# Kernel optimization log

Hardware: AMD Instinct MI355X
Metric: run time of the kernel (lower is better)

Reference implementation:

```python
import jax, jax.numpy as jnp
import numpy as np

N, E = 20000, 320000
IN_F, EF, H, C = 2, 1, 128, 2
BN_S = 1.0 / float(np.sqrt(1.0 + 1e-5))  # eval-mode BatchNorm1d with running mean 0, var 1


def _gated_gcn_conv(h, e, src, dst, p, act, residual):
    # DGL GatedGCNConv: e' = C e + D h_src + E h_dst;
    # h' = A h + sum_{in-edges} sigmoid(e') * B h_src / (sum sigmoid(e') + 1e-6)
    Aw, Ab, Bw, Bb, Cw, Cb, Dw, Db, Ew, Eb, bhg, bhb, beg, beb = p
    h_in, e_in = h, e
    Ah = h @ Aw + Ab
    Bh = h @ Bw + Bb
    Dh = h @ Dw + Db
    Eh = h @ Ew + Eb
    e2 = e @ Cw + Cb + Dh[src] + Eh[dst]          # [E, H]
    sig = jax.nn.sigmoid(e2)
    num = jax.ops.segment_sum(sig * Bh[src], dst, num_segments=N)  # [N, H]
    den = jax.ops.segment_sum(sig, dst, num_segments=N)            # [N, H]
    h2 = Ah + num / (den + 1e-6)
    # BatchNorm (eval): (x - 0)/sqrt(1 + eps) * gamma + beta
    h2 = bhg * (h2 * BN_S) + bhb
    e2 = beg * (e2 * BN_S) + beb
    h2, e2 = act(h2), act(e2)
    if residual:
        h2 = h2 + h_in
        e2 = e2 + e_in
    return h2, e2


def _forward(node_feats, edge_feats, src, dst, P):
    (a0_w, a0_b, b0_w, b0_b, c0_w, c0_b, d0_w, d0_b, e0_w, e0_b,
     bnh0_g, bnh0_b, bne0_g, bne0_b,
     aL_w, aL_b, bL_w, bL_b, cL_w, cL_b, dL_w, dL_b, eL_w, eL_b,
     bnhL_g, bnhL_b, bneL_g, bneL_b,
     mlp_w1, mlp_b1, mlp_w2, mlp_b2) = P
    h, e = node_feats, edge_feats
    # layer 0: elu inside conv, residual off (2->128, 1->128)
    p0 = (a0_w, a0_b, b0_w, b0_b, c0_w, c0_b, d0_w, d0_b, e0_w, e0_b,
          bnh0_g, bnh0_b, bne0_g, bne0_b)
    h, e = _gated_gcn_conv(h, e, src, dst, p0, jax.nn.elu, residual=False)
    h = jax.nn.leaky_relu(h)
    e = jax.nn.leaky_relu(e)
    # layers 1..2: leaky_relu inside conv, residual on (128->128)
    for l in range(2):
        pl = (aL_w[l], aL_b[l], bL_w[l], bL_b[l], cL_w[l], cL_b[l],
              dL_w[l], dL_b[l], eL_w[l], eL_b[l],
              bnhL_g[l], bnhL_b[l], bneL_g[l], bneL_b[l])
        h, e = _gated_gcn_conv(h, e, src, dst, pl, jax.nn.leaky_relu, residual=True)
        h = jax.nn.leaky_relu(h)
        e = jax.nn.leaky_relu(e)
    # edge classifier: gather endpoints, concat with edge feats, MLP
    edge_repr = jnp.concatenate([h[src], h[dst], e], axis=1)  # [E, 3H]
    hid = jax.nn.relu(edge_repr @ mlp_w1 + mlp_b1)
    return hid @ mlp_w2 + mlp_b2                               # [E, C]


PARAM_NAMES = ["a0_w", "a0_b", "b0_w", "b0_b", "c0_w", "c0_b", "d0_w", "d0_b",
               "e0_w", "e0_b", "bnh0_g", "bnh0_b", "bne0_g", "bne0_b",
               "aL_w", "aL_b", "bL_w", "bL_b", "cL_w", "cL_b", "dL_w", "dL_b",
               "eL_w", "eL_b", "bnhL_g", "bnhL_b", "bneL_g", "bneL_b",
               "mlp_w1", "mlp_b1", "mlp_w2", "mlp_b2"]


def setup_inputs() -> dict:
    key = jax.random.key(0)
    ks = iter(jax.random.split(key, 64))
    nrm = lambda shp: jax.random.normal(next(ks), shp, dtype=jnp.float32) * 0.05
    inp = {}
    inp["node_feats"] = jax.random.normal(next(ks), (N, IN_F), dtype=jnp.float32)
    inp["edge_feats"] = jax.random.normal(next(ks), (E, EF), dtype=jnp.float32)
    inp["src"] = jax.random.randint(next(ks), (E,), 0, N, dtype=jnp.int32)
    inp["dst"] = jax.random.randint(next(ks), (E,), 0, N, dtype=jnp.int32)
    # layer 0 linears (A,B,D,E: in->H; C: edge->H), biases zero-init like common practice
    for nm, din in [("a0", IN_F), ("b0", IN_F), ("c0", EF), ("d0", IN_F), ("e0", IN_F)]:
        inp[nm + "_w"] = nrm((din, H))
        inp[nm + "_b"] = nrm((H,))
    inp["bnh0_g"] = jnp.ones((H,), jnp.float32)
    inp["bnh0_b"] = jnp.zeros((H,), jnp.float32)
    inp["bne0_g"] = jnp.ones((H,), jnp.float32)
    inp["bne0_b"] = jnp.zeros((H,), jnp.float32)
    # layers 1..2 stacked
    for nm in ["aL", "bL", "cL", "dL", "eL"]:
        inp[nm + "_w"] = nrm((2, H, H))
        inp[nm + "_b"] = nrm((2, H))
    inp["bnhL_g"] = jnp.ones((2, H), jnp.float32)
    inp["bnhL_b"] = jnp.zeros((2, H), jnp.float32)
    inp["bneL_g"] = jnp.ones((2, H), jnp.float32)
    inp["bneL_b"] = jnp.zeros((2, H), jnp.float32)
    # edge MLP
    inp["mlp_w1"] = nrm((3 * H, H))
    inp["mlp_b1"] = nrm((H,))
    inp["mlp_w2"] = nrm((H, C))
    inp["mlp_b2"] = nrm((C,))
    return inp


def reference(node_feats, edge_feats, src, dst,
              a0_w, a0_b, b0_w, b0_b, c0_w, c0_b, d0_w, d0_b, e0_w, e0_b,
              bnh0_g, bnh0_b, bne0_g, bne0_b,
              aL_w, aL_b, bL_w, bL_b, cL_w, cL_b, dL_w, dL_b, eL_w, eL_b,
              bnhL_g, bnhL_b, bneL_g, bneL_b,
              mlp_w1, mlp_b1, mlp_w2, mlp_b2):
    P = (a0_w, a0_b, b0_w, b0_b, c0_w, c0_b, d0_w, d0_b, e0_w, e0_b,
         bnh0_g, bnh0_b, bne0_g, bne0_b,
         aL_w, aL_b, bL_w, bL_b, cL_w, cL_b, dL_w, dL_b, eL_w, eL_b,
         bnhL_g, bnhL_b, bneL_g, bneL_b,
         mlp_w1, mlp_b1, mlp_w2, mlp_b2)
    return _forward(node_feats, edge_feats, src, dst, P)
```

## Files before the change

kernel.cpp:

```cpp
#include <hip/hip_runtime.h>
#include <hip/hip_bf16.h>
#include <math.h>

#define NN 20000
#define NE 320000
#define H 128
#define NH (NN * H)

typedef short bf16x8 __attribute__((ext_vector_type(8)));
typedef float f32x4 __attribute__((ext_vector_type(4)));
typedef unsigned short u16x8 __attribute__((ext_vector_type(8)));

__device__ __forceinline__ float lrelu(float x) { return x > 0.f ? x : 0.01f * x; }
__device__ __forceinline__ float eluf(float x)  { return x > 0.f ? x : expm1f(x); }
__device__ __forceinline__ float sigf(float x)  { return 1.f / (1.f + __expf(-x)); }
__device__ __forceinline__ unsigned short f2b(float x) {
    __hip_bfloat16 h = __float2bfloat16(x);
    return *reinterpret_cast<unsigned short*>(&h);
}
__device__ __forceinline__ float b2f(unsigned short u) {
    __hip_bfloat16 h = *reinterpret_cast<__hip_bfloat16*>(&u);
    return __bfloat162float(h);
}
#define BN_S 0.99999500003749973f

struct PackPtrs { const float* w[13]; };
__global__ __launch_bounds__(256) void k_pack(PackPtrs p, unsigned short* __restrict__ dst) {
    int gid = blockIdx.x * 256 + threadIdx.x;
    int m = gid >> 11;
    int r = gid & 2047;
    int t = r >> 8, kk = (r >> 6) & 3, lane = r & 63;
    const float* W = p.w[m];
    int col = t * 16 + (lane & 15);
    int krow = kk * 32 + (lane >> 4) * 8;
    unsigned short* o = dst + (size_t)m * 16384 + (size_t)r * 8;
#pragma unroll
    for (int j = 0; j < 8; ++j) o[j] = f2b(W[(krow + j) * H + col]);
}

__global__ __launch_bounds__(256) void k_deg(const int* __restrict__ dst, int* __restrict__ deg) {
    int e = blockIdx.x * 256 + threadIdx.x;
    if (e < NE) atomicAdd(&deg[dst[e]], 1);
}

__global__ __launch_bounds__(256) void k_scan(const int* __restrict__ deg,
                                              int* __restrict__ off, int* __restrict__ cursor) {
    __shared__ int sums[256];
    const int t = threadIdx.x;
    const int per = (NN + 255) / 256;
    const int base = t * per;
    int s = 0;
    for (int i = 0; i < per; ++i) { int idx = base + i; if (idx < NN) s += deg[idx]; }
    sums[t] = s;
    __syncthreads();
    for (int d = 1; d < 256; d <<= 1) {
        int v = (t >= d) ? sums[t - d] : 0;
        __syncthreads();
        sums[t] += v;
        __syncthreads();
    }
    int run = (t == 0) ? 0 : sums[t - 1];
    for (int i = 0; i < per; ++i) {
        int idx = base + i;
        if (idx < NN) { off[idx] = run; cursor[idx] = run; run += deg[idx]; }
    }
}

__global__ __launch_bounds__(256) void k_fill(const int* __restrict__ dst,
                                              int* __restrict__ cursor, int* __restrict__ csr) {
    int e = blockIdx.x * 256 + threadIdx.x;
    if (e < NE) {
        int pos = atomicAdd(&cursor[dst[e]], 1);
        csr[pos] = e;
    }
}

__global__ __launch_bounds__(256) void k_seqs(const int* __restrict__ csr,
                                              const int* __restrict__ src,
                                              const int* __restrict__ dst,
                                              int* __restrict__ srcseq,
                                              int* __restrict__ dstseq) {
    int pos = blockIdx.x * 256 + threadIdx.x;
    if (pos < NE) {
        int eid = csr[pos];
        srcseq[pos] = src[eid];
        dstseq[pos] = dst[eid];
    }
}

__global__ __launch_bounds__(256) void k_nodelin0(
        const float* __restrict__ nf,
        const float* __restrict__ wa, const float* __restrict__ ba,
        const float* __restrict__ wb, const float* __restrict__ bb,
        const float* __restrict__ wd, const float* __restrict__ bd,
        const float* __restrict__ we, const float* __restrict__ be,
        float* __restrict__ lin) {
    int idx = blockIdx.x * 256 + threadIdx.x;
    int n = idx >> 7, c = idx & 127;
    float x0 = nf[n * 2], x1 = nf[n * 2 + 1];
    lin[0 * NH + idx] = fmaf(x0, wa[c], fmaf(x1, wa[128 + c], ba[c]));
    lin[1 * NH + idx] = fmaf(x0, wb[c], fmaf(x1, wb[128 + c], bb[c]));
    lin[2 * NH + idx] = fmaf(x0, wd[c], fmaf(x1, wd[128 + c], bd[c]));
    lin[3 * NH + idx] = fmaf(x0, we[c], fmaf(x1, we[128 + c], be[c]));
}

__global__ __launch_bounds__(256) void k_edge0(
        const float* __restrict__ ef,
        const float* __restrict__ cw, const float* __restrict__ cb,
        const int* __restrict__ src, const int* __restrict__ dst,
        const float* __restrict__ lin,
        const float* __restrict__ g, const float* __restrict__ bt,
        unsigned short* __restrict__ ebuf) {
    const int tid = threadIdx.x;
    const int e  = blockIdx.x * 8 + (tid >> 5);
    const int c0 = (tid & 31) * 4;
    const int s = src[e], d = dst[e];
    const float ev = ef[e];
    const float4 cw4 = *(const float4*)(cw + c0);
    const float4 cb4 = *(const float4*)(cb + c0);
    const float4 Dh  = *(const float4*)(lin + 2 * NH + (size_t)s * H + c0);
    const float4 Eh  = *(const float4*)(lin + 3 * NH + (size_t)d * H + c0);
    const float4 g4  = *(const float4*)(g + c0);
    const float4 bt4 = *(const float4*)(bt + c0);
    float e2[4] = { fmaf(ev, cw4.x, cb4.x) + Dh.x + Eh.x,
                    fmaf(ev, cw4.y, cb4.y) + Dh.y + Eh.y,
                    fmaf(ev, cw4.z, cb4.z) + Dh.z + Eh.z,
                    fmaf(ev, cw4.w, cb4.w) + Dh.w + Eh.w };
    const float gg[4] = { g4.x, g4.y, g4.z, g4.w };
    const float bb[4] = { bt4.x, bt4.y, bt4.z, bt4.w };
    ushort4 u;
    u.x = f2b(lrelu(eluf(fmaf(gg[0], e2[0] * BN_S, bb[0]))));
    u.y = f2b(lrelu(eluf(fmaf(gg[1], e2[1] * BN_S, bb[1]))));
    u.z = f2b(lrelu(eluf(fmaf(gg[2], e2[2] * BN_S, bb[2]))));
    u.w = f2b(lrelu(eluf(fmaf(gg[3], e2[3] * BN_S, bb[3]))));
    *(ushort4*)(ebuf + (size_t)e * H + c0) = u;
}

__global__ __launch_bounds__(256) void k_agg0(
        const int* __restrict__ off, const int* __restrict__ deg,
        const int* __restrict__ csr, const int* __restrict__ srcseq,
        const float* __restrict__ ef, const float* __restrict__ cw, const float* __restrict__ cb,
        const float* __restrict__ lin,
        const float* __restrict__ g, const float* __restrict__ bt,
        float* __restrict__ hout, unsigned short* __restrict__ hbout) {
    const int tid = threadIdx.x;
    const int n = blockIdx.x * 2 + (tid >> 7);
    const int c = tid & 127;
    const int base = off[n], dg = deg[n];
    float num = 0.f, den = 0.f;
    const float Ehn = lin[3 * NH + (size_t)n * H + c];
    const float cwc = cw[c], cbc = cb[c];
    int i = 0;
    for (; i + 4 <= dg; i += 4) {
        int e0 = csr[base + i],     e1 = csr[base + i + 1];
        int e2_ = csr[base + i + 2], e3 = csr[base + i + 3];
        int s0 = srcseq[base + i],     s1 = srcseq[base + i + 1];
        int s2 = srcseq[base + i + 2], s3 = srcseq[base + i + 3];
        float x0 = fmaf(ef[e0], cwc, cbc) + lin[2 * NH + (size_t)s0 * H + c] + Ehn;
        float x1 = fmaf(ef[e1], cwc, cbc) + lin[2 * NH + (size_t)s1 * H + c] + Ehn;
        float x2 = fmaf(ef[e2_], cwc, cbc) + lin[2 * NH + (size_t)s2 * H + c] + Ehn;
        float x3 = fmaf(ef[e3], cwc, cbc) + lin[2 * NH + (size_t)s3 * H + c] + Ehn;
        float g0 = sigf(x0), g1 = sigf(x1), g2 = sigf(x2), g3 = sigf(x3);
        num = fmaf(g0, lin[1 * NH + (size_t)s0 * H + c], num); den += g0;
        num = fmaf(g1, lin[1 * NH + (size_t)s1 * H + c], num); den += g1;
        num = fmaf(g2, lin[1 * NH + (size_t)s2 * H + c], num); den += g2;
        num = fmaf(g3, lin[1 * NH + (size_t)s3 * H + c], num); den += g3;
    }
    for (; i < dg; ++i) {
        int ea = csr[base + i];
        int sa = srcseq[base + i];
        float xa = fmaf(ef[ea], cwc, cbc) + lin[2 * NH + (size_t)sa * H + c] + Ehn;
        float ga = sigf(xa);
        num = fmaf(ga, lin[1 * NH + (size_t)sa * H + c], num); den += ga;
    }
    float h2 = lin[(size_t)n * H + c] + num / (den + 1e-6f);
    h2 = fmaf(g[c], h2 * BN_S, bt[c]);
    h2 = eluf(h2);
    float r = lrelu(h2);
    hout[(size_t)n * H + c] = r;
    hbout[(size_t)n * H + c] = f2b(r);
}

__global__ __launch_bounds__(256) void k_agg(
        const int* __restrict__ off, const int* __restrict__ deg,
        const int* __restrict__ srcseq,
        const unsigned short* __restrict__ e2seq,
        const float* __restrict__ lin,
        const float* __restrict__ g, const float* __restrict__ bt,
        const float* __restrict__ hin, float* __restrict__ hout,
        unsigned short* __restrict__ hbout) {
    const int tid = threadIdx.x;
    const int n = blockIdx.x * 2 + (tid >> 7);
    const int c = tid & 127;
    const int base = off[n], dg = deg[n];
    float num = 0.f, den = 0.f;
    int i = 0;
    for (; i + 4 <= dg; i += 4) {
        int s0 = srcseq[base + i],     s1 = srcseq[base + i + 1];
        int s2 = srcseq[base + i + 2], s3 = srcseq[base + i + 3];
        float x0 = b2f(e2seq[(size_t)(base + i) * H + c]);
        float x1 = b2f(e2seq[(size_t)(base + i + 1) * H + c]);
        float x2 = b2f(e2seq[(size_t)(base + i + 2) * H + c]);
        float x3 = b2f(e2seq[(size_t)(base + i + 3) * H + c]);
        float g0 = sigf(x0), g1 = sigf(x1), g2 = sigf(x2), g3 = sigf(x3);
        num = fmaf(g0, lin[1 * NH + (size_t)s0 * H + c], num); den += g0;
        num = fmaf(g1, lin[1 * NH + (size_t)s1 * H + c], num); den += g1;
        num = fmaf(g2, lin[1 * NH + (size_t)s2 * H + c], num); den += g2;
        num = fmaf(g3, lin[1 * NH + (size_t)s3 * H + c], num); den += g3;
    }
    for (; i < dg; ++i) {
        int sa = srcseq[base + i];
        float xa = b2f(e2seq[(size_t)(base + i) * H + c]);
        float ga = sigf(xa);
        num = fmaf(ga, lin[1 * NH + (size_t)sa * H + c], num); den += ga;
    }
    float h2 = lin[(size_t)n * H + c] + num / (den + 1e-6f);
    h2 = fmaf(g[c], h2 * BN_S, bt[c]);
    h2 = lrelu(h2);
    h2 += hin[(size_t)n * H + c];
    float r = lrelu(h2);
    hout[(size_t)n * H + c] = r;
    hbout[(size_t)n * H + c] = f2b(r);
}

__global__ __launch_bounds__(256) void k_nodegemm(
        const unsigned short* __restrict__ hb,
        const unsigned short* __restrict__ wpack,
        const float* __restrict__ ba, const float* __restrict__ bb,
        const float* __restrict__ bd, const float* __restrict__ be,
        float* __restrict__ lin) {
    __shared__ __align__(16) unsigned short AT[64][136];
    const int tid = threadIdx.x;
    const int nbase = blockIdx.x * 64;
    const int which = blockIdx.y;
    const unsigned short* Wp = wpack + (size_t)which * 16384;
    const float* B = which == 0 ? ba : which == 1 ? bb : which == 2 ? bd : be;
#pragma unroll
    for (int rep = 0; rep < 4; ++rep) {
        int flat = (rep * 256 + tid) * 8;
        int r = flat >> 7, k0 = flat & 127;
        int n = nbase + r;
        u16x8 v = {};
        if (n < NN) v = *(const u16x8*)(hb + (size_t)n * H + k0);
        *(u16x8*)(&AT[r][k0]) = v;
    }
    __syncthreads();
    const int lane = tid & 63, wave = tid >> 6;
    const int lrow = lane & 15, quad = lane >> 4;
    f32x4 acc[8] = {};
#pragma unroll
    for (int kk = 0; kk < 4; ++kk) {
        bf16x8 af = *(const bf16x8*)(&AT[wave * 16 + lrow][kk * 32 + quad * 8]);
#pragma unroll
        for (int t = 0; t < 8; ++t) {
            bf16x8 bfv = *(const bf16x8*)(Wp + ((t * 4 + kk) * 64 + lane) * 8);
            acc[t] = __builtin_amdgcn_mfma_f32_16x16x32_bf16(af, bfv, acc[t], 0, 0, 0);
        }
    }
#pragma unroll
    for (int t = 0; t < 8; ++t) {
        int col = t * 16 + lrow;
        float bv = B[col];
#pragma unroll
        for (int reg = 0; reg < 4; ++reg) {
            int n = nbase + wave * 16 + quad * 4 + reg;
            if (n < NN)
                lin[(size_t)which * NH + (size_t)n * H + col] = acc[t][reg] + bv;
        }
    }
}

__global__ __launch_bounds__(256) void k_pgemm(
        const unsigned short* __restrict__ hb,
        const unsigned short* __restrict__ w1p,
        const float* __restrict__ b1,
        float* __restrict__ P) {
    __shared__ __align__(16) unsigned short AT[64][136];
    const int tid = threadIdx.x;
    const int nbase = blockIdx.x * 64;
    const int y = blockIdx.y;
    const unsigned short* Wp = w1p + (size_t)y * 16384;
#pragma unroll
    for (int rep = 0; rep < 4; ++rep) {
        int flat = (rep * 256 + tid) * 8;
        int r = flat >> 7, k0 = flat & 127;
        int n = nbase + r;
        u16x8 v = {};
        if (n < NN) v = *(const u16x8*)(hb + (size_t)n * H + k0);
        *(u16x8*)(&AT[r][k0]) = v;
    }
    __syncthreads();
    const int lane = tid & 63, wave = tid >> 6;
    const int lrow = lane & 15, quad = lane >> 4;
    f32x4 acc[8] = {};
#pragma unroll
    for (int kk = 0; kk < 4; ++kk) {
        bf16x8 af = *(const bf16x8*)(&AT[wave * 16 + lrow][kk * 32 + quad * 8]);
#pragma unroll
        for (int t = 0; t < 8; ++t) {
            bf16x8 bfv = *(const bf16x8*)(Wp + ((t * 4 + kk) * 64 + lane) * 8);
            acc[t] = __builtin_amdgcn_mfma_f32_16x16x32_bf16(af, bfv, acc[t], 0, 0, 0);
        }
    }
#pragma unroll
    for (int t = 0; t < 8; ++t) {
        int col = t * 16 + lrow;
        float bv = (y == 0) ? b1[col] : 0.f;
#pragma unroll
        for (int reg = 0; reg < 4; ++reg) {
            int n = nbase + wave * 16 + quad * 4 + reg;
            if (n < NN)
                P[(size_t)y * NH + (size_t)n * H + col] = acc[t][reg] + bv;
        }
    }
}

__global__ __launch_bounds__(256) void k_edgegemm(
        unsigned short* __restrict__ ebuf,
        unsigned short* __restrict__ e2seq,
        const unsigned short* __restrict__ Wp,
        const float* __restrict__ cb,
        const int* __restrict__ csr,
        const int* __restrict__ srcseq, const int* __restrict__ dstseq,
        const float* __restrict__ lin,
        const float* __restrict__ g, const float* __restrict__ bt) {
    __shared__ __align__(16) unsigned short AT[64][136];
    const int tid = threadIdx.x;
    const int ebase = blockIdx.x * 64;
#pragma unroll
    for (int rep = 0; rep < 4; ++rep) {
        int flat = (rep * 256 + tid) * 8;
        int r = flat >> 7, k0 = flat & 127;
        int eid = csr[ebase + r];
        *(u16x8*)(&AT[r][k0]) = *(const u16x8*)(ebuf + (size_t)eid * H + k0);
    }
    __syncthreads();
    const int lane = tid & 63, wave = tid >> 6;
    const int lrow = lane & 15, quad = lane >> 4;
    f32x4 acc[8] = {};
#pragma unroll
    for (int kk = 0; kk < 4; ++kk) {
        bf16x8 af = *(const bf16x8*)(&AT[wave * 16 + lrow][kk * 32 + quad * 8]);
#pragma unroll
        for (int t = 0; t < 8; ++t) {
            bf16x8 bfv = *(const bf16x8*)(Wp + ((t * 4 + kk) * 64 + lane) * 8);
            acc[t] = __builtin_amdgcn_mfma_f32_16x16x32_bf16(af, bfv, acc[t], 0, 0, 0);
        }
    }
    const int r0 = ebase + wave * 16 + quad * 4;
    const int rr0 = wave * 16 + quad * 4;
    int eid[4], sv[4], dv[4];
#pragma unroll
    for (int reg = 0; reg < 4; ++reg) {
        eid[reg] = csr[r0 + reg];
        sv[reg]  = srcseq[r0 + reg];
        dv[reg]  = dstseq[r0 + reg];
    }
#pragma unroll
    for (int t = 0; t < 8; ++t) {
        int col = t * 16 + lrow;
        float cbv = cb[col], gv = g[col], btv = bt[col];
#pragma unroll
        for (int reg = 0; reg < 4; ++reg) {
            float Dh = lin[2 * NH + (size_t)sv[reg] * H + col];
            float Eh = lin[3 * NH + (size_t)dv[reg] * H + col];
            float e2 = acc[t][reg] + cbv + Dh + Eh;
            e2seq[(size_t)(r0 + reg) * H + col] = f2b(e2);
            float tt = lrelu(fmaf(gv, e2 * BN_S, btv));
            float ein = b2f(AT[rr0 + reg][col]);
            ebuf[(size_t)eid[reg] * H + col] = f2b(lrelu(tt + ein));
        }
    }
}

__global__ __launch_bounds__(256) void k_mlp2(
        const unsigned short* __restrict__ ebuf,
        const float* __restrict__ P,
        const int* __restrict__ src, const int* __restrict__ dst,
        const unsigned short* __restrict__ w1p2,
        const float* __restrict__ w2, const float* __restrict__ b2,
        float* __restrict__ out) {
    __shared__ __align__(16) unsigned short AT[64][136];
    const int tid = threadIdx.x;
    const int ebase = blockIdx.x * 64;
#pragma unroll
    for (int rep = 0; rep < 4; ++rep) {
        int flat = (rep * 256 + tid) * 8;
        int r = flat >> 7, k0 = flat & 127;
        *(u16x8*)(&AT[r][k0]) = *(const u16x8*)(ebuf + (size_t)(ebase + r) * H + k0);
    }
    __syncthreads();
    const int lane = tid & 63, wave = tid >> 6;
    const int lrow = lane & 15, quad = lane >> 4;
    f32x4 acc[8] = {};
#pragma unroll
    for (int kk = 0; kk < 4; ++kk) {
        bf16x8 af = *(const bf16x8*)(&AT[wave * 16 + lrow][kk * 32 + quad * 8]);
#pragma unroll
        for (int t = 0; t < 8; ++t) {
            bf16x8 bfv = *(const bf16x8*)(w1p2 + ((t * 4 + kk) * 64 + lane) * 8);
            acc[t] = __builtin_amdgcn_mfma_f32_16x16x32_bf16(af, bfv, acc[t], 0, 0, 0);
        }
    }
    const int e0 = ebase + wave * 16 + quad * 4;
    const float b20 = b2[0], b21 = b2[1];
#pragma unroll
    for (int reg = 0; reg < 4; ++reg) {
        const int e = e0 + reg;
        const int s = src[e], d = dst[e];
        float p1v[8], p2v[8];
#pragma unroll
        for (int t = 0; t < 8; ++t) {
            int col = t * 16 + lrow;
            p1v[t] = P[(size_t)s * H + col];
            p2v[t] = P[(size_t)NH + (size_t)d * H + col];
        }
        float p0 = 0.f, p1 = 0.f;
#pragma unroll
        for (int t = 0; t < 8; ++t) {
            int col = t * 16 + lrow;
            float hv = fmaxf(acc[t][reg] + p1v[t] + p2v[t], 0.f);
            p0 = fmaf(hv, w2[col * 2], p0);
            p1 = fmaf(hv, w2[col * 2 + 1], p1);
        }
#pragma unroll
        for (int off = 8; off; off >>= 1) {
            p0 += __shfl_xor(p0, off, 16);
            p1 += __shfl_xor(p1, off, 16);
        }
        if (lrow == 0) {
            out[e * 2]     = p0 + b20;
            out[e * 2 + 1] = p1 + b21;
        }
    }
}

extern "C" void kernel_launch(void* const* d_in, const int* in_sizes, int n_in,
                              void* d_out, int out_size, void* d_ws, size_t ws_size,
                              hipStream_t stream) {
    const float* nf  = (const float*)d_in[0];
    const float* ef  = (const float*)d_in[1];
    const int*   src = (const int*)d_in[2];
    const int*   dst = (const int*)d_in[3];
    const float *a0w = (const float*)d_in[4],  *a0b = (const float*)d_in[5];
    const float *b0w = (const float*)d_in[6],  *b0b = (const float*)d_in[7];
    const float *c0w = (const float*)d_in[8],  *c0b = (const float*)d_in[9];
    const float *d0w = (const float*)d_in[10], *d0b = (const float*)d_in[11];
    const float *e0w = (const float*)d_in[12], *e0b = (const float*)d_in[13];
    const float *bnh0g = (const float*)d_in[14], *bnh0b = (const float*)d_in[15];
    const float *bne0g = (const float*)d_in[16], *bne0b = (const float*)d_in[17];
    const float *aLw = (const float*)d_in[18], *aLb = (const float*)d_in[19];
    const float *bLw = (const float*)d_in[20], *bLb = (const float*)d_in[21];
    const float *cLw = (const float*)d_in[22], *cLb = (const float*)d_in[23];
    const float *dLw = (const float*)d_in[24], *dLb = (const float*)d_in[25];
    const float *eLw = (const float*)d_in[26], *eLb = (const float*)d_in[27];
    const float *bnhLg = (const float*)d_in[28], *bnhLb = (const float*)d_in[29];
    const float *bneLg = (const float*)d_in[30], *bneLb = (const float*)d_in[31];
    const float *w1 = (const float*)d_in[32], *b1 = (const float*)d_in[33];
    const float *w2 = (const float*)d_in[34], *b2 = (const float*)d_in[35];
    float* out = (float*)d_out;

    char* ws = (char*)d_ws;
    unsigned short* ebuf  = (unsigned short*)ws;
    unsigned short* e2seq = ebuf + (size_t)NE * H;
    float* lin = (float*)(e2seq + (size_t)NE * H);
    float* h0  = lin + 4ull * NH;
    float* h1  = h0 + NH;
    unsigned short* hb0 = (unsigned short*)(h1 + NH);
    unsigned short* hb1 = hb0 + NH;
    int* deg    = (int*)(hb1 + NH);
    int* off    = deg + NN;
    int* cursor = off + NN;
    int* csr    = cursor + NN;
    int* srcseq = csr + NE;
    int* dstseq = srcseq + NE;
    unsigned short* wpack = (unsigned short*)(dstseq + NE);
    float* P = (float*)e2seq;

    PackPtrs pp;
    const size_t HH = (size_t)H * H;
    for (int l = 0; l < 2; ++l) {
        pp.w[l * 5 + 0] = aLw + l * HH;
        pp.w[l * 5 + 1] = bLw + l * HH;
        pp.w[l * 5 + 2] = dLw + l * HH;
        pp.w[l * 5 + 3] = eLw + l * HH;
        pp.w[l * 5 + 4] = cLw + l * HH;
    }
    pp.w[10] = w1; pp.w[11] = w1 + HH; pp.w[12] = w1 + 2 * HH;
    k_pack<<<104, 256, 0, stream>>>(pp, wpack);

    hipMemsetAsync(deg, 0, NN * sizeof(int), stream);
    k_deg<<<(NE + 255) / 256, 256, 0, stream>>>(dst, deg);
    k_scan<<<1, 256, 0, stream>>>(deg, off, cursor);
    k_fill<<<(NE + 255) / 256, 256, 0, stream>>>(dst, cursor, csr);
    k_seqs<<<(NE + 255) / 256, 256, 0, stream>>>(csr, src, dst, srcseq, dstseq);

    k_nodelin0<<<NN * H / 256, 256, 0, stream>>>(nf, a0w, a0b, b0w, b0b, d0w, d0b, e0w, e0b, lin);
    k_edge0<<<NE / 8, 256, 0, stream>>>(ef, c0w, c0b, src, dst, lin, bne0g, bne0b, ebuf);
    k_agg0<<<NN / 2, 256, 0, stream>>>(off, deg, csr, srcseq, ef, c0w, c0b,
                                       lin, bnh0g, bnh0b, h0, hb0);

    for (int l = 0; l < 2; ++l) {
        const float* hin = (l == 0) ? h0 : h1;
        float* hout      = (l == 0) ? h1 : h0;
        const unsigned short* hbin = (l == 0) ? hb0 : hb1;
        unsigned short* hbout      = (l == 0) ? hb1 : hb0;
        k_nodegemm<<<dim3(313, 4), 256, 0, stream>>>(hbin,
            wpack + (size_t)l * 5 * 16384,
            aLb + l * H, bLb + l * H, dLb + l * H, eLb + l * H, lin);
        k_edgegemm<<<NE / 64, 256, 0, stream>>>(ebuf, e2seq,
                                                wpack + (size_t)(l * 5 + 4) * 16384,
                                                cLb + l * H, csr, srcseq, dstseq, lin,
                                                bneLg + l * H, bneLb + l * H);
        k_agg<<<NN / 2, 256, 0, stream>>>(off, deg, srcseq, e2seq,
                                          lin, bnhLg + l * H, bnhLb + l * H,
                                          hin, hout, hbout);
    }

    k_pgemm<<<dim3(313, 2), 256, 0, stream>>>(hb0, wpack + 10ull * 16384, b1, P);
    k_mlp2<<<NE / 64, 256, 0, stream>>>(ebuf, P, src, dst, wpack + 12ull * 16384,
                                        w2, b2, out);

    (void)in_sizes; (void)n_in; (void)out_size; (void)ws_size;
}
```

Measured before the change: 692.6 us.

## Store edge features in CSR-sorted order to remove indirect edge indexing

New measurement: 666.5 us. 1.04x faster.

```diff
diff --git a/kernel.cpp b/kernel.cpp
--- a/kernel.cpp
+++ b/kernel.cpp
@@ -78,13 +78,16 @@
 __global__ __launch_bounds__(256) void k_seqs(const int* __restrict__ csr,
                                               const int* __restrict__ src,
                                               const int* __restrict__ dst,
+                                              const float* __restrict__ ef,
                                               int* __restrict__ srcseq,
-                                              int* __restrict__ dstseq) {
+                                              int* __restrict__ dstseq,
+                                              float* __restrict__ efseq) {
     int pos = blockIdx.x * 256 + threadIdx.x;
     if (pos < NE) {
         int eid = csr[pos];
         srcseq[pos] = src[eid];
         dstseq[pos] = dst[eid];
+        efseq[pos]  = ef[eid];
     }
 }
 
@@ -105,17 +108,17 @@
 }
 
 __global__ __launch_bounds__(256) void k_edge0(
-        const float* __restrict__ ef,
+        const float* __restrict__ efseq,
         const float* __restrict__ cw, const float* __restrict__ cb,
-        const int* __restrict__ src, const int* __restrict__ dst,
+        const int* __restrict__ srcseq, const int* __restrict__ dstseq,
         const float* __restrict__ lin,
         const float* __restrict__ g, const float* __restrict__ bt,
         unsigned short* __restrict__ ebuf) {
     const int tid = threadIdx.x;
-    const int e  = blockIdx.x * 8 + (tid >> 5);
+    const int pos = blockIdx.x * 8 + (tid >> 5);
     const int c0 = (tid & 31) * 4;
-    const int s = src[e], d = dst[e];
-    const float ev = ef[e];
+    const int s = srcseq[pos], d = dstseq[pos];
+    const float ev = efseq[pos];
     const float4 cw4 = *(const float4*)(cw + c0);
     const float4 cb4 = *(const float4*)(cb + c0);
     const float4 Dh  = *(const float4*)(lin + 2 * NH + (size_t)s * H + c0);
@@ -133,13 +136,13 @@
     u.y = f2b(lrelu(eluf(fmaf(gg[1], e2[1] * BN_S, bb[1]))));
     u.z = f2b(lrelu(eluf(fmaf(gg[2], e2[2] * BN_S, bb[2]))));
     u.w = f2b(lrelu(eluf(fmaf(gg[3], e2[3] * BN_S, bb[3]))));
-    *(ushort4*)(ebuf + (size_t)e * H + c0) = u;
+    *(ushort4*)(ebuf + (size_t)pos * H + c0) = u;
 }
 
 __global__ __launch_bounds__(256) void k_agg0(
         const int* __restrict__ off, const int* __restrict__ deg,
-        const int* __restrict__ csr, const int* __restrict__ srcseq,
-        const float* __restrict__ ef, const float* __restrict__ cw, const float* __restrict__ cb,
+        const int* __restrict__ srcseq, const float* __restrict__ efseq,
+        const float* __restrict__ cw, const float* __restrict__ cb,
         const float* __restrict__ lin,
         const float* __restrict__ g, const float* __restrict__ bt,
         float* __restrict__ hout, unsigned short* __restrict__ hbout) {
@@ -152,14 +155,12 @@
     const float cwc = cw[c], cbc = cb[c];
     int i = 0;
     for (; i + 4 <= dg; i += 4) {
-        int e0 = csr[base + i],     e1 = csr[base + i + 1];
-        int e2_ = csr[base + i + 2], e3 = csr[base + i + 3];
         int s0 = srcseq[base + i],     s1 = srcseq[base + i + 1];
         int s2 = srcseq[base + i + 2], s3 = srcseq[base + i + 3];
-        float x0 = fmaf(ef[e0], cwc, cbc) + lin[2 * NH + (size_t)s0 * H + c] + Ehn;
-        float x1 = fmaf(ef[e1], cwc, cbc) + lin[2 * NH + (size_t)s1 * H + c] + Ehn;
-        float x2 = fmaf(ef[e2_], cwc, cbc) + lin[2 * NH + (size_t)s2 * H + c] + Ehn;
-        float x3 = fmaf(ef[e3], cwc, cbc) + lin[2 * NH + (size_t)s3 * H + c] + Ehn;
+        float x0 = fmaf(efseq[base + i],     cwc, cbc) + lin[2 * NH + (size_t)s0 * H + c] + Ehn;
+        float x1 = fmaf(efseq[base + i + 1], cwc, cbc) + lin[2 * NH + (size_t)s1 * H + c] + Ehn;
+        float x2 = fmaf(efseq[base + i + 2], cwc, cbc) + lin[2 * NH + (size_t)s2 * H + c] + Ehn;
+        float x3 = fmaf(efseq[base + i + 3], cwc, cbc) + lin[2 * NH + (size_t)s3 * H + c] + Ehn;
         float g0 = sigf(x0), g1 = sigf(x1), g2 = sigf(x2), g3 = sigf(x3);
         num = fmaf(g0, lin[1 * NH + (size_t)s0 * H + c], num); den += g0;
         num = fmaf(g1, lin[1 * NH + (size_t)s1 * H + c], num); den += g1;
@@ -167,9 +168,8 @@
         num = fmaf(g3, lin[1 * NH + (size_t)s3 * H + c], num); den += g3;
     }
     for (; i < dg; ++i) {
-        int ea = csr[base + i];
         int sa = srcseq[base + i];
-        float xa = fmaf(ef[ea], cwc, cbc) + lin[2 * NH + (size_t)sa * H + c] + Ehn;
+        float xa = fmaf(efseq[base + i], cwc, cbc) + lin[2 * NH + (size_t)sa * H + c] + Ehn;
         float ga = sigf(xa);
         num = fmaf(ga, lin[1 * NH + (size_t)sa * H + c], num); den += ga;
     }
@@ -320,7 +320,6 @@
         unsigned short* __restrict__ e2seq,
         const unsigned short* __restrict__ Wp,
         const float* __restrict__ cb,
-        const int* __restrict__ csr,
         const int* __restrict__ srcseq, const int* __restrict__ dstseq,
         const float* __restrict__ lin,
         const float* __restrict__ g, const float* __restrict__ bt) {
@@ -331,8 +330,7 @@
     for (int rep = 0; rep < 4; ++rep) {
         int flat = (rep * 256 + tid) * 8;
         int r = flat >> 7, k0 = flat & 127;
-        int eid = csr[ebase + r];
-        *(u16x8*)(&AT[r][k0]) = *(const u16x8*)(ebuf + (size_t)eid * H + k0);
+        *(u16x8*)(&AT[r][k0]) = *(const u16x8*)(ebuf + (size_t)(ebase + r) * H + k0);
     }
     __syncthreads();
     const int lane = tid & 63, wave = tid >> 6;
@@ -349,12 +347,11 @@
     }
     const int r0 = ebase + wave * 16 + quad * 4;
     const int rr0 = wave * 16 + quad * 4;
-    int eid[4], sv[4], dv[4];
+    int sv[4], dv[4];
 #pragma unroll
     for (int reg = 0; reg < 4; ++reg) {
-        eid[reg] = csr[r0 + reg];
-        sv[reg]  = srcseq[r0 + reg];
-        dv[reg]  = dstseq[r0 + reg];
+        sv[reg] = srcseq[r0 + reg];
+        dv[reg] = dstseq[r0 + reg];
     }
 #pragma unroll
     for (int t = 0; t < 8; ++t) {
@@ -368,7 +365,7 @@
             e2seq[(size_t)(r0 + reg) * H + col] = f2b(e2);
             float tt = lrelu(fmaf(gv, e2 * BN_S, btv));
             float ein = b2f(AT[rr0 + reg][col]);
-            ebuf[(size_t)eid[reg] * H + col] = f2b(lrelu(tt + ein));
+            ebuf[(size_t)(r0 + reg) * H + col] = f2b(lrelu(tt + ein));
         }
     }
 }
@@ -376,7 +373,8 @@
 __global__ __launch_bounds__(256) void k_mlp2(
         const unsigned short* __restrict__ ebuf,
         const float* __restrict__ P,
-        const int* __restrict__ src, const int* __restrict__ dst,
+        const int* __restrict__ csr,
+        const int* __restrict__ srcseq, const int* __restrict__ dstseq,
         const unsigned short* __restrict__ w1p2,
         const float* __restrict__ w2, const float* __restrict__ b2,
         float* __restrict__ out) {
@@ -407,7 +405,7 @@
 #pragma unroll
     for (int reg = 0; reg < 4; ++reg) {
         const int e = e0 + reg;
-        const int s = src[e], d = dst[e];
+        const int s = srcseq[e], d = dstseq[e];
         float p1v[8], p2v[8];
 #pragma unroll
         for (int t = 0; t < 8; ++t) {
@@ -429,8 +427,9 @@
             p1 += __shfl_xor(p1, off, 16);
         }
         if (lrow == 0) {
-            out[e * 2]     = p0 + b20;
-            out[e * 2 + 1] = p1 + b21;
+            int eid = csr[e];
+            out[eid * 2]     = p0 + b20;
+            out[eid * 2 + 1] = p1 + b21;
         }
     }
 }
@@ -474,7 +473,8 @@
     int* csr    = cursor + NN;
     int* srcseq = csr + NE;
     int* dstseq = srcseq + NE;
-    unsigned short* wpack = (unsigned short*)(dstseq + NE);
+    float* efseq = (float*)(dstseq + NE);
+    unsigned short* wpack = (unsigned short*)(efseq + NE);
     float* P = (float*)e2seq;
 
     PackPtrs pp;
@@ -493,11 +493,12 @@
     k_deg<<<(NE + 255) / 256, 256, 0, stream>>>(dst, deg);
     k_scan<<<1, 256, 0, stream>>>(deg, off, cursor);
     k_fill<<<(NE + 255) / 256, 256, 0, stream>>>(dst, cursor, csr);
-    k_seqs<<<(NE + 255) / 256, 256, 0, stream>>>(csr, src, dst, srcseq, dstseq);
+    k_seqs<<<(NE + 255) / 256, 256, 0, stream>>>(csr, src, dst, ef, srcseq, dstseq, efseq);
 
     k_nodelin0<<<NN * H / 256, 256, 0, stream>>>(nf, a0w, a0b, b0w, b0b, d0w, d0b, e0w, e0b, lin);
-    k_edge0<<<NE / 8, 256, 0, stream>>>(ef, c0w, c0b, src, dst, lin, bne0g, bne0b, ebuf);
-    k_agg0<<<NN / 2, 256, 0, stream>>>(off, deg, csr, srcseq, ef, c0w, c0b,
+    k_edge0<<<NE / 8, 256, 0, stream>>>(efseq, c0w, c0b, srcseq, dstseq, lin,
+                                        bne0g, bne0b, ebuf);
+    k_agg0<<<NN / 2, 256, 0, stream>>>(off, deg, srcseq, efseq, c0w, c0b,
                                        lin, bnh0g, bnh0b, h0, hb0);
 
     for (int l = 0; l < 2; ++l) {
@@ -510,7 +511,7 @@
             aLb + l * H, bLb + l * H, dLb + l * H, eLb + l * H, lin);
         k_edgegemm<<<NE / 64, 256, 0, stream>>>(ebuf, e2seq,
                                                 wpack + (size_t)(l * 5 + 4) * 16384,
-                                                cLb + l * H, csr, srcseq, dstseq, lin,
+                                                cLb + l * H, srcseq, dstseq, lin,
                                                 bneLg + l * H, bneLb + l * H);
         k_agg<<<NN / 2, 256, 0, stream>>>(off, deg, srcseq, e2seq,
                                           lin, bnhLg + l * H, bnhLb + l * H,
@@ -518,8 +519,8 @@
     }
 
     k_pgemm<<<dim3(313, 2), 256, 0, stream>>>(hb0, wpack + 10ull * 16384, b1, P);
-    k_mlp2<<<NE / 64, 256, 0, stream>>>(ebuf, P, src, dst, wpack + 12ull * 16384,
-                                        w2, b2, out);
+    k_mlp2<<<NE / 64, 256, 0, stream>>>(ebuf, P, csr, srcseq, dstseq,
+                                        wpack + 12ull * 16384, w2, b2, out);
 
     (void)in_sizes; (void)n_in; (void)out_size; (void)ws_size;
 }
```
